# Optimization experiments

Measured on AMD Instinct MI355X. Metric: run time of the kernel, lower is better.

The kernel has to match this reference:

```python
import jax, jax.numpy as jnp
import numpy as np

BETA = 0.95
THR = 1.0
NUM_STEPS = 100
ALPHA = 2.0  # snntorch atan surrogate default

@jax.custom_vjp
def atan_spike(x):
    return (x > 0).astype(x.dtype)

def _as_fwd(x):
    return (x > 0).astype(x.dtype), x

def _as_bwd(x, g):
    return (g * (ALPHA / 2) / (1 + (jnp.pi / 2 * ALPHA * x) ** 2),)

atan_spike.defvjp(_as_fwd, _as_bwd)


def setup_inputs() -> dict:
    key = jax.random.key(0)
    ks = jax.random.split(key, 9)
    B = 16384
    SH, NH, CO, OUT = 1024, 1024, 256, 64
    s = 0.05
    return {
        "x": jax.random.normal(ks[0], (B, 105), jnp.float32),
        "snn_w1": jax.random.normal(ks[1], (SH, 5), jnp.float32) * s,
        "snn_b1": jnp.zeros((SH,), jnp.float32),
        "snn_w2": jax.random.normal(ks[2], (OUT, SH), jnp.float32) * s,
        "snn_b2": jnp.zeros((OUT,), jnp.float32),
        "nn_w1": jax.random.normal(ks[3], (NH, 5), jnp.float32) * s,
        "nn_b1": jnp.zeros((NH,), jnp.float32),
        "nn_w2": jax.random.normal(ks[4], (OUT, NH), jnp.float32) * s,
        "nn_b2": jnp.zeros((OUT,), jnp.float32),
        "conv_w": jax.random.normal(ks[5], (32, 1, 3), jnp.float32) * s,
        "conv_b": jnp.zeros((32,), jnp.float32),
        "cnn_fc_w": jax.random.normal(ks[6], (CO, 32 * 50), jnp.float32) * s,
        "cnn_fc_b": jnp.zeros((CO,), jnp.float32),
        "comb_w": jax.random.normal(ks[7], (OUT, 2 * OUT + CO), jnp.float32) * s,
        "comb_b": jnp.zeros((OUT,), jnp.float32),
    }


def _forward(x, snn_w1, snn_b1, snn_w2, snn_b2, nn_w1, nn_b1, nn_w2, nn_b2,
             conv_w, conv_b, cnn_fc_w, cnn_fc_b, comb_w, comb_b):
    feats = x[:, :5]                 # [B,5]
    wave = x[:, 5:][:, None, :]      # [B,1,100]
    B = x.shape[0]

    # ---- SNN branch (LIF, beta leak, subtract reset, threshold 1.0) ----
    cur1 = feats @ snn_w1.T + snn_b1  # input current is constant across steps

    def step(carry, _):
        mem1, spk1, mem2, spk2 = carry
        # reset term uses detached spike (snntorch mem_reset detaches)
        mem1 = BETA * mem1 + cur1 - jax.lax.stop_gradient(spk1) * THR
        spk1 = atan_spike(mem1 - THR)
        cur2 = spk1 @ snn_w2.T + snn_b2
        mem2 = BETA * mem2 + cur2 - jax.lax.stop_gradient(spk2) * THR
        spk2 = atan_spike(mem2 - THR)
        return (mem1, spk1, mem2, spk2), spk2

    z1 = jnp.zeros_like(cur1)
    z2 = jnp.zeros((B, snn_w2.shape[0]), cur1.dtype)
    _, spk_rec = jax.lax.scan(step, (z1, z1, z2, z2), None, length=NUM_STEPS)
    snn_out = spk_rec.mean(axis=0)   # [B,OUT]

    # ---- MLP branch ----
    nn_out = jax.nn.relu(feats @ nn_w1.T + nn_b1) @ nn_w2.T + nn_b2

    # ---- CNN branch ----
    c = jax.lax.conv_general_dilated(wave, conv_w, (1,), [(1, 1)],
                                     dimension_numbers=("NCW", "OIW", "NCW"))
    c = jax.nn.relu(c + conv_b[None, :, None])   # [B,32,100]
    c = c.reshape(B, 32, 50, 2).max(axis=-1)      # MaxPool1d(k=2,s=2)
    cnn_out = c.reshape(B, -1) @ cnn_fc_w.T + cnn_fc_b

    combined = jnp.concatenate([snn_out, nn_out, cnn_out], axis=1)
    return combined @ comb_w.T + comb_b


def reference(x, snn_w1, snn_b1, snn_w2, snn_b2, nn_w1, nn_b1, nn_w2, nn_b2,
              conv_w, conv_b, cnn_fc_w, cnn_fc_b, comb_w, comb_b):
    return _forward(x, snn_w1, snn_b1, snn_w2, snn_b2, nn_w1, nn_b1, nn_w2,
                    nn_b2, conv_w, conv_b, cnn_fc_w, cnn_fc_b, comb_w, comb_b)
```

## Files before the change

kernel.cpp:

```cpp
#include <hip/hip_runtime.h>

typedef __bf16 bf16x8_t __attribute__((ext_vector_type(8)));
typedef float f32x4_t __attribute__((ext_vector_type(4)));
typedef float f32x2_t __attribute__((ext_vector_type(2)));

#define NSTEPS 100
#define COMBF 51200u

static __device__ __forceinline__ unsigned short f2bfu(float v) {
  union { __bf16 h; unsigned short u; } c; c.h = (__bf16)v; return c.u;
}
static __device__ __forceinline__ unsigned int pack2bf(float a, float b) {
  return (unsigned)f2bfu(a) | ((unsigned)f2bfu(b) << 16);
}
union BF8U { unsigned int u[4]; bf16x8_t v; };

static __device__ __forceinline__ void pk_mul_ip(f32x2_t &a, f32x2_t b) {
  asm("v_pk_mul_f32 %0, %0, %1" : "+v"(a) : "v"(b));
}
static __device__ __forceinline__ void pk_add_ip(f32x2_t &a, f32x2_t b) {
  asm("v_pk_add_f32 %0, %0, %1" : "+v"(a) : "v"(b));
}

static __device__ __forceinline__ bf16x8_t bfrag_f32(const float* __restrict__ p, float s) {
  BF8U r;
#pragma unroll
  for (int i = 0; i < 4; ++i) r.u[i] = pack2bf(p[2*i]*s, p[2*i+1]*s);
  return r.v;
}

static __device__ __forceinline__ void comb_store(unsigned char* ldsp, int k, int row, float v) {
  *(unsigned short*)(ldsp + COMBF +
      (unsigned)((k >> 5)*1024 + (((k >> 3) & 3)*16 + row)*16 + (k & 7)*2)) = f2bfu(v);
}

__global__ __launch_bounds__(512, 2)
void hybrid_v6(const float* __restrict__ x,
               const float* __restrict__ snn_w1, const float* __restrict__ snn_b1,
               const float* __restrict__ snn_w2, const float* __restrict__ snn_b2,
               const float* __restrict__ nn_w1,  const float* __restrict__ nn_b1,
               const float* __restrict__ nn_w2,  const float* __restrict__ nn_b2,
               const float* __restrict__ conv_w, const float* __restrict__ conv_b,
               const float* __restrict__ fc_w,   const float* __restrict__ fc_b,
               const float* __restrict__ comb_w, const float* __restrict__ comb_b,
               const unsigned short* __restrict__ fcwb, int use_bf,
               float* __restrict__ out)
{
  __shared__ __align__(16) unsigned char lds[131072];
  const int tid  = threadIdx.x;
  const int w    = tid >> 6;
  const int l    = tid & 63;
  const int q    = l >> 4;
  const int m    = l & 15;
  const int row0 = blockIdx.x * 16;

  const int hi  = w >> 2;
  const int ntr = w & 3;
  const int rn  = ntr*16 + m;
  const int rA  = hi*4 + q;

  const float* xr = x + (row0 + m)*105;
  const float f0 = xr[0], f1 = xr[1], f2 = xr[2], f3 = xr[3], f4 = xr[4];
  const float b2l = snn_b2[rn];

  bf16x8_t bfr[4][4];
#pragma unroll
  for (int ci = 0; ci < 4; ++ci)
#pragma unroll
    for (int nt = 0; nt < 4; ++nt)
      bfr[ci][nt] = bfrag_f32(snn_w2 + (nt*16 + m)*1024 + (w*4 + ci)*32 + q*8, 1.f);

  f32x2_t c2[16], mem2[16];
  f32x2_t beta2; beta2.x = 0.95f; beta2.y = 0.95f;
  {
    const int kb = w*128 + q*8;
#pragma unroll
    for (int ci = 0; ci < 4; ++ci) {
      const float* wp = snn_w1 + (kb + ci*32)*5;
      float wa[40];
#pragma unroll
      for (int u2 = 0; u2 < 10; ++u2) {
        const float4 t4 = *(const float4*)(wp + u2*4);
        wa[u2*4+0] = t4.x; wa[u2*4+1] = t4.y; wa[u2*4+2] = t4.z; wa[u2*4+3] = t4.w;
      }
      float cc[8];
#pragma unroll
      for (int j = 0; j < 8; ++j)
        cc[j] = f0*wa[j*5] + f1*wa[j*5+1] + f2*wa[j*5+2] + f3*wa[j*5+3] + f4*wa[j*5+4]
              + snn_b1[kb + ci*32 + j];
#pragma unroll
      for (int jj = 0; jj < 4; ++jj) {
        f32x2_t t; t.x = cc[2*jj]; t.y = cc[2*jj+1];
        c2[ci*4+jj] = t;
        f32x2_t z; z.x = 0.f; z.y = 0.f;
        mem2[ci*4+jj] = z;
      }
    }
  }

  BF8U afr[4][4];
#pragma unroll
  for (int ci = 0; ci < 4; ++ci)
#pragma unroll
    for (int j = 0; j < 4; ++j) afr[3][ci].u[j] = 0u;

  auto lif_step = [&](int pi, int po) {
#pragma unroll
    for (int i = 0; i < 16; ++i) {
      const unsigned pw = afr[pi][i>>2].u[i&3];
      f32x2_t sn;
      sn.x = __uint_as_float((pw << 16) | 0x80000000u);
      sn.y = __uint_as_float((pw & 0x3F800000u) | 0x80000000u);
      pk_mul_ip(mem2[i], beta2);
      pk_add_ip(mem2[i], c2[i]);
      pk_add_ip(mem2[i], sn);
      const unsigned lo  = mem2[i].x > 1.f ? 0x3F80u     : 0u;
      const unsigned hi2 = mem2[i].y > 1.f ? 0x3F800000u : 0u;
      afr[po][i>>2].u[i&3] = lo | hi2;
    }
  };
  lif_step(3,0); lif_step(0,1); lif_step(1,2); lif_step(2,3);

  f32x2_t m2;     m2.x = 0.f;      m2.y = 0.f;
  f32x2_t s2neg;  s2neg.x = -0.0f; s2neg.y = -0.0f;
  f32x2_t cntneg; cntneg.x = 0.f;  cntneg.y = 0.f;
  f32x2_t sbias2; sbias2.x = b2l;  sbias2.y = b2l;

  const unsigned wbase = (unsigned)(w*4096 + (q&1)*2048 + (q>>1)*4 + m*8);
  const unsigned rbase = (unsigned)(rA*512 + rn*8);
  const f32x4_t z4 = {0.f, 0.f, 0.f, 0.f};

  auto reduce_lif2 = [&](f32x2_t v[8]) {
    pk_add_ip(v[0], v[1]); pk_add_ip(v[2], v[3]);
    pk_add_ip(v[4], v[5]); pk_add_ip(v[6], v[7]);
    pk_add_ip(v[0], v[2]); pk_add_ip(v[4], v[6]);
    pk_add_ip(v[0], v[4]);
    pk_add_ip(v[0], sbias2);
    pk_mul_ip(m2, beta2);
    pk_add_ip(m2, v[0]);
    pk_add_ip(m2, s2neg);
    s2neg.x = m2.x > 1.f ? -1.0f : -0.0f;
    s2neg.y = m2.y > 1.f ? -1.0f : -0.0f;
    pk_add_ip(cntneg, s2neg);
  };

#pragma unroll 1
  for (int ss = 0; ss < 25; ++ss) {
#pragma unroll
    for (int k = 0; k < 4; ++k) {
      f32x4_t acc[4] = {z4, z4, z4, z4};
#pragma unroll
      for (int ci = 0; ci < 4; ++ci)
#pragma unroll
        for (int nt = 0; nt < 4; ++nt)
          acc[nt] = __builtin_amdgcn_mfma_f32_16x16x32_bf16(afr[k][ci].v, bfr[ci][nt], acc[nt], 0,0,0);
      unsigned char* wp = lds + (unsigned)(k*32768) + wbase;
#pragma unroll
      for (int nt = 0; nt < 4; ++nt)
#pragma unroll
        for (int r = 0; r < 4; ++r)
          *(float*)(wp + (unsigned)(r*512 + nt*128)) = acc[nt][r];
    }
    __syncthreads();

    {
      const unsigned char* rp = lds + rbase;
      f32x2_t va[8], vb[8];
#pragma unroll
      for (int s = 0; s < 8; ++s) va[s] = *(const f32x2_t*)(rp + (unsigned)(s*4096));
#pragma unroll
      for (int s = 0; s < 8; ++s) vb[s] = *(const f32x2_t*)(rp + 32768u + (unsigned)(s*4096));
      if (ss < 24) { lif_step(3,0); lif_step(0,1); lif_step(1,2); lif_step(2,3); }
      reduce_lif2(va);
      reduce_lif2(vb);
#pragma unroll
      for (int s = 0; s < 8; ++s) va[s] = *(const f32x2_t*)(rp + 65536u + (unsigned)(s*4096));
#pragma unroll
      for (int s = 0; s < 8; ++s) vb[s] = *(const f32x2_t*)(rp + 98304u + (unsigned)(s*4096));
      reduce_lif2(va);
      reduce_lif2(vb);
    }
    __syncthreads();
  }

#pragma unroll
  for (int ci = 0; ci < 4; ++ci)
#pragma unroll
    for (int nt = 0; nt < 4; ++nt)
      bfr[ci][nt] = bfrag_f32(nn_w2 + (nt*16 + m)*1024 + (w*4 + ci)*32 + q*8, 1.f);
  {
    BF8U hfr[4];
    const int kb = w*128 + q*8;
#pragma unroll
    for (int ci = 0; ci < 4; ++ci) {
      const float* wp = nn_w1 + (kb + ci*32)*5;
      float wa[40];
#pragma unroll
      for (int u2 = 0; u2 < 10; ++u2) {
        const float4 t4 = *(const float4*)(wp + u2*4);
        wa[u2*4+0] = t4.x; wa[u2*4+1] = t4.y; wa[u2*4+2] = t4.z; wa[u2*4+3] = t4.w;
      }
      float hv[8];
#pragma unroll
      for (int j = 0; j < 8; ++j) {
        const float h = f0*wa[j*5] + f1*wa[j*5+1] + f2*wa[j*5+2] + f3*wa[j*5+3] + f4*wa[j*5+4]
                      + nn_b1[kb + ci*32 + j];
        hv[j] = fmaxf(h, 0.f);
      }
#pragma unroll
      for (int jj = 0; jj < 4; ++jj) hfr[ci].u[jj] = pack2bf(hv[2*jj], hv[2*jj+1]);
    }
    f32x4_t acc[4] = {z4, z4, z4, z4};
#pragma unroll
    for (int ci = 0; ci < 4; ++ci)
#pragma unroll
      for (int nt = 0; nt < 4; ++nt)
        acc[nt] = __builtin_amdgcn_mfma_f32_16x16x32_bf16(hfr[ci].v, bfr[ci][nt], acc[nt], 0,0,0);
#pragma unroll
    for (int nt = 0; nt < 4; ++nt)
#pragma unroll
      for (int r = 0; r < 4; ++r)
        *(float*)(lds + wbase + (unsigned)(r*512 + nt*128)) = acc[nt][r];
  }
  __syncthreads();
  {
    f32x2_t va[8];
    const unsigned char* rp = lds + rbase;
#pragma unroll
    for (int s = 0; s < 8; ++s) va[s] = *(const f32x2_t*)(rp + (unsigned)(s*4096));
    pk_add_ip(va[0], va[1]); pk_add_ip(va[2], va[3]);
    pk_add_ip(va[4], va[5]); pk_add_ip(va[6], va[7]);
    pk_add_ip(va[0], va[2]); pk_add_ip(va[4], va[6]);
    pk_add_ip(va[0], va[4]);
    const float nb = nn_b2[rn];
    f32x2_t nb2; nb2.x = nb; nb2.y = nb;
    pk_add_ip(va[0], nb2);
    comb_store(lds, rn,      rA,     cntneg.x * -0.0078125f);
    comb_store(lds, rn,      rA + 8, cntneg.y * -0.0078125f);
    comb_store(lds, 64 + rn, rA,     va[0].x);
    comb_store(lds, 64 + rn, rA + 8, va[0].y);
  }
  __syncthreads();

  {
    const int ch = tid >> 4;
    const float cw0 = conv_w[ch*3+0], cw1 = conv_w[ch*3+1], cw2 = conv_w[ch*3+2];
    const float cbb = conv_b[ch];
    const float* xw = xr + 5;
    float xm1 = 0.f, x0v = xw[0];
#pragma unroll 1
    for (int p = 0; p < 50; ++p) {
      const float xp1 = xw[2*p + 1];
      const float xp2 = (p < 49) ? xw[2*p + 2] : 0.f;
      const float av = cw0*xm1 + cw1*x0v + cw2*xp1 + cbb;
      const float bv = cw0*x0v + cw1*xp1 + cw2*xp2 + cbb;
      const float pv = fmaxf(fmaxf(av, 0.f), fmaxf(bv, 0.f));
      const int k = ch*50 + p;
      *(unsigned short*)(lds + (unsigned)((k>>5)*1024 + (((k>>3)&3)*16 + m)*16 + (k&7)*2)) = f2bfu(pv);
      xm1 = xp1; x0v = xp2;
    }
  }
  __syncthreads();

  {
    const int c0 = (w*2 + 0)*16 + m;
    const int c1 = (w*2 + 1)*16 + m;
    f32x4_t e0 = z4, o0 = z4, e1 = z4, o1 = z4;
    if (use_bf) {
#pragma unroll 2
      for (int kc = 0; kc < 50; kc += 2) {
        const bf16x8_t a0 = *(const bf16x8_t*)(lds + (unsigned)((kc*64 + l)*16));
        const bf16x8_t a1 = *(const bf16x8_t*)(lds + (unsigned)(((kc+1)*64 + l)*16));
        e0 = __builtin_amdgcn_mfma_f32_16x16x32_bf16(a0, *(const bf16x8_t*)(fcwb + c0*1600 + kc*32 + q*8), e0, 0,0,0);
        o0 = __builtin_amdgcn_mfma_f32_16x16x32_bf16(a1, *(const bf16x8_t*)(fcwb + c0*1600 + (kc+1)*32 + q*8), o0, 0,0,0);
        e1 = __builtin_amdgcn_mfma_f32_16x16x32_bf16(a0, *(const bf16x8_t*)(fcwb + c1*1600 + kc*32 + q*8), e1, 0,0,0);
        o1 = __builtin_amdgcn_mfma_f32_16x16x32_bf16(a1, *(const bf16x8_t*)(fcwb + c1*1600 + (kc+1)*32 + q*8), o1, 0,0,0);
      }
    } else {
#pragma unroll 2
      for (int kc = 0; kc < 50; kc += 2) {
        const bf16x8_t a0 = *(const bf16x8_t*)(lds + (unsigned)((kc*64 + l)*16));
        const bf16x8_t a1 = *(const bf16x8_t*)(lds + (unsigned)(((kc+1)*64 + l)*16));
        e0 = __builtin_amdgcn_mfma_f32_16x16x32_bf16(a0, bfrag_f32(fc_w + c0*1600 + kc*32 + q*8, 1.f), e0, 0,0,0);
        o0 = __builtin_amdgcn_mfma_f32_16x16x32_bf16(a1, bfrag_f32(fc_w + c0*1600 + (kc+1)*32 + q*8, 1.f), o0, 0,0,0);
        e1 = __builtin_amdgcn_mfma_f32_16x16x32_bf16(a0, bfrag_f32(fc_w + c1*1600 + kc*32 + q*8, 1.f), e1, 0,0,0);
        o1 = __builtin_amdgcn_mfma_f32_16x16x32_bf16(a1, bfrag_f32(fc_w + c1*1600 + (kc+1)*32 + q*8, 1.f), o1, 0,0,0);
      }
    }
    const float fb0 = fc_b[c0], fb1 = fc_b[c1];
#pragma unroll
    for (int r = 0; r < 4; ++r) {
      comb_store(lds, 128 + c0, q*4 + r, (e0[r] + o0[r]) + fb0);
      comb_store(lds, 128 + c1, q*4 + r, (e1[r] + o1[r]) + fb1);
    }
  }
  __syncthreads();

  if (w < 4) {
    const int cn = w*16 + m;
    f32x4_t oe = z4, oo = z4;
#pragma unroll
    for (int kc = 0; kc < 12; kc += 2) {
      const bf16x8_t a0 = *(const bf16x8_t*)(lds + COMBF + (unsigned)((kc*64 + l)*16));
      const bf16x8_t a1 = *(const bf16x8_t*)(lds + COMBF + (unsigned)(((kc+1)*64 + l)*16));
      const float s0 = (kc    < 2) ? 1.28f : 1.f;
      const float s1 = (kc+1 < 2) ? 1.28f : 1.f;
      oe = __builtin_amdgcn_mfma_f32_16x16x32_bf16(a0, bfrag_f32(comb_w + cn*384 + kc*32 + q*8, s0), oe, 0,0,0);
      oo = __builtin_amdgcn_mfma_f32_16x16x32_bf16(a1, bfrag_f32(comb_w + cn*384 + (kc+1)*32 + q*8, s1), oo, 0,0,0);
    }
    const float cb2 = comb_b[cn];
#pragma unroll
    for (int r = 0; r < 4; ++r)
      out[(row0 + q*4 + r)*64 + cn] = (oe[r] + oo[r]) + cb2;
  }
}

__global__ __launch_bounds__(256)
void fcw_to_bf16(const float* __restrict__ src, unsigned short* __restrict__ dst) {
  const int i = (blockIdx.x * 256 + threadIdx.x) * 4;
  const float4 v = *(const float4*)(src + i);
  ushort4 o;
  o.x = f2bfu(v.x); o.y = f2bfu(v.y); o.z = f2bfu(v.z); o.w = f2bfu(v.w);
  *(ushort4*)(dst + i) = o;
}

extern "C" void kernel_launch(void* const* d_in, const int* in_sizes, int n_in,
                              void* d_out, int out_size, void* d_ws, size_t ws_size,
                              hipStream_t stream) {
  const float* x       = (const float*)d_in[0];
  const float* snn_w1  = (const float*)d_in[1];
  const float* snn_b1  = (const float*)d_in[2];
  const float* snn_w2  = (const float*)d_in[3];
  const float* snn_b2  = (const float*)d_in[4];
  const float* nn_w1   = (const float*)d_in[5];
  const float* nn_b1   = (const float*)d_in[6];
  const float* nn_w2   = (const float*)d_in[7];
  const float* nn_b2   = (const float*)d_in[8];
  const float* conv_w  = (const float*)d_in[9];
  const float* conv_b  = (const float*)d_in[10];
  const float* fc_w    = (const float*)d_in[11];
  const float* fc_b    = (const float*)d_in[12];
  const float* comb_w  = (const float*)d_in[13];
  const float* comb_b  = (const float*)d_in[14];
  float* outp = (float*)d_out;

  const int rows = in_sizes[0] / 105;
  const int grid = rows / 16;

  const size_t fcw_elems = (size_t)in_sizes[11];
  const int use_bf = (ws_size >= fcw_elems * 2) ? 1 : 0;
  unsigned short* fcwb = (unsigned short*)d_ws;
  if (use_bf) {
    fcw_to_bf16<<<dim3((unsigned)(fcw_elems / 1024)), dim3(256), 0, stream>>>(fc_w, fcwb);
  }

  hybrid_v6<<<dim3(grid), dim3(512), 0, stream>>>(
      x, snn_w1, snn_b1, snn_w2, snn_b2,
      nn_w1, nn_b1, nn_w2, nn_b2,
      conv_w, conv_b, fc_w, fc_b, comb_w, comb_b,
      fcwb, use_bf, outp);
}
```

Baseline: 762.9 us.

## Interleave layer-1 LIF step with each MFMA step to cut register footprint

Replaces the four-deep buffer of precomputed layer-1 spike fragments with a single fragment set. The next LIF step now runs right after each step's MFMAs instead of four steps being batched in the reduction phase. Spike state is kept as negative float reset values and packed to bf16 with a perm instruction. This frees VGPRs and lets the VALU LIF work overlap the MFMA latency, but the inner k loop is no longer unrolled, which adds loop overhead and restricts scheduling.

```diff
diff --git a/kernel.cpp b/kernel.cpp
--- a/kernel.cpp
+++ b/kernel.cpp
@@ -35,7 +35,7 @@
 }
 
 __global__ __launch_bounds__(512, 2)
-void hybrid_v6(const float* __restrict__ x,
+void hybrid_v7(const float* __restrict__ x,
                const float* __restrict__ snn_w1, const float* __restrict__ snn_b1,
                const float* __restrict__ snn_w2, const float* __restrict__ snn_b2,
                const float* __restrict__ nn_w1,  const float* __restrict__ nn_b1,
@@ -70,7 +70,7 @@
     for (int nt = 0; nt < 4; ++nt)
       bfr[ci][nt] = bfrag_f32(snn_w2 + (nt*16 + m)*1024 + (w*4 + ci)*32 + q*8, 1.f);
 
-  f32x2_t c2[16], mem2[16];
+  f32x2_t c2[16], mem2[16], spneg2[16];
   f32x2_t beta2; beta2.x = 0.95f; beta2.y = 0.95f;
   {
     const int kb = w*128 + q*8;
@@ -94,32 +94,29 @@
         c2[ci*4+jj] = t;
         f32x2_t z; z.x = 0.f; z.y = 0.f;
         mem2[ci*4+jj] = z;
-      }
-    }
-  }
-
-  BF8U afr[4][4];
-#pragma unroll
-  for (int ci = 0; ci < 4; ++ci)
-#pragma unroll
-    for (int j = 0; j < 4; ++j) afr[3][ci].u[j] = 0u;
-
-  auto lif_step = [&](int pi, int po) {
+        f32x2_t nz; nz.x = -0.0f; nz.y = -0.0f;
+        spneg2[ci*4+jj] = nz;
+      }
+    }
+  }
+
+  BF8U afr[4];
+  auto lif_step = [&]() {
 #pragma unroll
     for (int i = 0; i < 16; ++i) {
-      const unsigned pw = afr[pi][i>>2].u[i&3];
-      f32x2_t sn;
-      sn.x = __uint_as_float((pw << 16) | 0x80000000u);
-      sn.y = __uint_as_float((pw & 0x3F800000u) | 0x80000000u);
       pk_mul_ip(mem2[i], beta2);
       pk_add_ip(mem2[i], c2[i]);
-      pk_add_ip(mem2[i], sn);
-      const unsigned lo  = mem2[i].x > 1.f ? 0x3F80u     : 0u;
-      const unsigned hi2 = mem2[i].y > 1.f ? 0x3F800000u : 0u;
-      afr[po][i>>2].u[i&3] = lo | hi2;
+      pk_add_ip(mem2[i], spneg2[i]);
+      f32x2_t sn;
+      sn.x = mem2[i].x > 1.f ? -1.0f : -0.0f;
+      sn.y = mem2[i].y > 1.f ? -1.0f : -0.0f;
+      spneg2[i] = sn;
+      afr[i>>2].u[i&3] =
+          __builtin_amdgcn_perm(__float_as_uint(sn.y), __float_as_uint(sn.x), 0x07060302u)
+          & 0x3F803F80u;
     }
   };
-  lif_step(3,0); lif_step(0,1); lif_step(1,2); lif_step(2,3);
+  lif_step();
 
   f32x2_t m2;     m2.x = 0.f;      m2.y = 0.f;
   f32x2_t s2neg;  s2neg.x = -0.0f; s2neg.y = -0.0f;
@@ -146,14 +143,15 @@
 
 #pragma unroll 1
   for (int ss = 0; ss < 25; ++ss) {
-#pragma unroll
+#pragma unroll 1
     for (int k = 0; k < 4; ++k) {
       f32x4_t acc[4] = {z4, z4, z4, z4};
 #pragma unroll
       for (int ci = 0; ci < 4; ++ci)
 #pragma unroll
         for (int nt = 0; nt < 4; ++nt)
-          acc[nt] = __builtin_amdgcn_mfma_f32_16x16x32_bf16(afr[k][ci].v, bfr[ci][nt], acc[nt], 0,0,0);
+          acc[nt] = __builtin_amdgcn_mfma_f32_16x16x32_bf16(afr[ci].v, bfr[ci][nt], acc[nt], 0,0,0);
+      if (ss*4 + k < NSTEPS - 1) lif_step();
       unsigned char* wp = lds + (unsigned)(k*32768) + wbase;
 #pragma unroll
       for (int nt = 0; nt < 4; ++nt)
@@ -170,7 +168,6 @@
       for (int s = 0; s < 8; ++s) va[s] = *(const f32x2_t*)(rp + (unsigned)(s*4096));
 #pragma unroll
       for (int s = 0; s < 8; ++s) vb[s] = *(const f32x2_t*)(rp + 32768u + (unsigned)(s*4096));
-      if (ss < 24) { lif_step(3,0); lif_step(0,1); lif_step(1,2); lif_step(2,3); }
       reduce_lif2(va);
       reduce_lif2(vb);
 #pragma unroll
@@ -354,7 +351,7 @@
     fcw_to_bf16<<<dim3((unsigned)(fcw_elems / 1024)), dim3(256), 0, stream>>>(fc_w, fcwb);
   }
 
-  hybrid_v6<<<dim3(grid), dim3(512), 0, stream>>>(
+  hybrid_v7<<<dim3(grid), dim3(512), 0, stream>>>(
       x, snn_w1, snn_b1, snn_w2, snn_b2,
       nn_w1, nn_b1, nn_w2, nn_b2,
       conv_w, conv_b, fc_w, fc_b, comb_w, comb_b,
```

After: 700.8 us. -8.1%, faster.

## Process two 16-row tiles per block and software-pipeline the SNN timestep loop

Applied to the files above, without the earlier changes.

Each block now handles 32 batch rows as two independent 16-row tiles (A and B), halving the grid. The SNN loop is restructured so each phase issues one timestep's MFMAs for both tiles, interleaves the next layer-1 LIF update and the reduction of the previous step's partials from a double-buffered LDS region, and uses one barrier per step instead of batching four steps with two barriers. This interleaving is meant to hide MFMA and LDS latency behind independent work and to reuse the weight fragments in registers across twice as many rows. In exchange it roughly doubles per-thread state (membrane and current registers), which raises register pressure and risks spills at the 512x2 launch bound. It also halves the number of blocks, which lowers parallelism across CUs.

```diff
diff --git a/kernel.cpp b/kernel.cpp
--- a/kernel.cpp
+++ b/kernel.cpp
@@ -5,7 +5,13 @@
 typedef float f32x2_t __attribute__((ext_vector_type(2)));
 
 #define NSTEPS 100
-#define COMBF 51200u
+#define APB0 0u
+#define APB1 32768u
+#define TB   65536u
+#define POOLA 0u
+#define POOLB 51200u
+#define COMBA 102400u
+#define COMBB 114688u
 
 static __device__ __forceinline__ unsigned short f2bfu(float v) {
   union { __bf16 h; unsigned short u; } c; c.h = (__bf16)v; return c.u;
@@ -29,22 +35,23 @@
   return r.v;
 }
 
-static __device__ __forceinline__ void comb_store(unsigned char* ldsp, int k, int row, float v) {
-  *(unsigned short*)(ldsp + COMBF +
+static __device__ __forceinline__ void comb_store(unsigned char* ldsp, unsigned base,
+                                                  int k, int row, float v) {
+  *(unsigned short*)(ldsp + base +
       (unsigned)((k >> 5)*1024 + (((k >> 3) & 3)*16 + row)*16 + (k & 7)*2)) = f2bfu(v);
 }
 
 __global__ __launch_bounds__(512, 2)
-void hybrid_v6(const float* __restrict__ x,
-               const float* __restrict__ snn_w1, const float* __restrict__ snn_b1,
-               const float* __restrict__ snn_w2, const float* __restrict__ snn_b2,
-               const float* __restrict__ nn_w1,  const float* __restrict__ nn_b1,
-               const float* __restrict__ nn_w2,  const float* __restrict__ nn_b2,
-               const float* __restrict__ conv_w, const float* __restrict__ conv_b,
-               const float* __restrict__ fc_w,   const float* __restrict__ fc_b,
-               const float* __restrict__ comb_w, const float* __restrict__ comb_b,
-               const unsigned short* __restrict__ fcwb, int use_bf,
-               float* __restrict__ out)
+void hybrid_v11(const float* __restrict__ x,
+                const float* __restrict__ snn_w1, const float* __restrict__ snn_b1,
+                const float* __restrict__ snn_w2, const float* __restrict__ snn_b2,
+                const float* __restrict__ nn_w1,  const float* __restrict__ nn_b1,
+                const float* __restrict__ nn_w2,  const float* __restrict__ nn_b2,
+                const float* __restrict__ conv_w, const float* __restrict__ conv_b,
+                const float* __restrict__ fc_w,   const float* __restrict__ fc_b,
+                const float* __restrict__ comb_w, const float* __restrict__ comb_b,
+                const unsigned short* __restrict__ fcwb, int use_bf,
+                float* __restrict__ out)
 {
   __shared__ __align__(16) unsigned char lds[131072];
   const int tid  = threadIdx.x;
@@ -52,15 +59,13 @@
   const int l    = tid & 63;
   const int q    = l >> 4;
   const int m    = l & 15;
-  const int row0 = blockIdx.x * 16;
+  const int row0 = blockIdx.x * 32;
 
   const int hi  = w >> 2;
   const int ntr = w & 3;
   const int rn  = ntr*16 + m;
   const int rA  = hi*4 + q;
 
-  const float* xr = x + (row0 + m)*105;
-  const float f0 = xr[0], f1 = xr[1], f2 = xr[2], f3 = xr[3], f4 = xr[4];
   const float b2l = snn_b2[rn];
 
   bf16x8_t bfr[4][4];
@@ -70,118 +75,177 @@
     for (int nt = 0; nt < 4; ++nt)
       bfr[ci][nt] = bfrag_f32(snn_w2 + (nt*16 + m)*1024 + (w*4 + ci)*32 + q*8, 1.f);
 
-  f32x2_t c2[16], mem2[16];
+  f32x2_t c2A[16], mem2A[16], c2B[16], mem2B[16];
   f32x2_t beta2; beta2.x = 0.95f; beta2.y = 0.95f;
   {
     const int kb = w*128 + q*8;
-#pragma unroll
-    for (int ci = 0; ci < 4; ++ci) {
-      const float* wp = snn_w1 + (kb + ci*32)*5;
-      float wa[40];
-#pragma unroll
-      for (int u2 = 0; u2 < 10; ++u2) {
-        const float4 t4 = *(const float4*)(wp + u2*4);
-        wa[u2*4+0] = t4.x; wa[u2*4+1] = t4.y; wa[u2*4+2] = t4.z; wa[u2*4+3] = t4.w;
-      }
-      float cc[8];
-#pragma unroll
-      for (int j = 0; j < 8; ++j)
-        cc[j] = f0*wa[j*5] + f1*wa[j*5+1] + f2*wa[j*5+2] + f3*wa[j*5+3] + f4*wa[j*5+4]
-              + snn_b1[kb + ci*32 + j];
-#pragma unroll
-      for (int jj = 0; jj < 4; ++jj) {
-        f32x2_t t; t.x = cc[2*jj]; t.y = cc[2*jj+1];
-        c2[ci*4+jj] = t;
-        f32x2_t z; z.x = 0.f; z.y = 0.f;
-        mem2[ci*4+jj] = z;
-      }
-    }
-  }
-
-  BF8U afr[4][4];
+    {
+      const float* xr = x + (row0 + m)*105;
+      const float f0 = xr[0], f1 = xr[1], f2 = xr[2], f3 = xr[3], f4 = xr[4];
+#pragma unroll
+      for (int ci = 0; ci < 4; ++ci) {
+        const float* wp = snn_w1 + (kb + ci*32)*5;
+        float wa[40];
+#pragma unroll
+        for (int u2 = 0; u2 < 10; ++u2) {
+          const float4 t4 = *(const float4*)(wp + u2*4);
+          wa[u2*4+0] = t4.x; wa[u2*4+1] = t4.y; wa[u2*4+2] = t4.z; wa[u2*4+3] = t4.w;
+        }
+        float cc[8];
+#pragma unroll
+        for (int j = 0; j < 8; ++j)
+          cc[j] = f0*wa[j*5] + f1*wa[j*5+1] + f2*wa[j*5+2] + f3*wa[j*5+3] + f4*wa[j*5+4]
+                + snn_b1[kb + ci*32 + j];
+#pragma unroll
+        for (int jj = 0; jj < 4; ++jj) {
+          f32x2_t t; t.x = cc[2*jj]; t.y = cc[2*jj+1];
+          c2A[ci*4+jj] = t;
+          f32x2_t z; z.x = 0.f; z.y = 0.f;
+          mem2A[ci*4+jj] = z;
+        }
+      }
+    }
+    {
+      const float* xr = x + (row0 + 16 + m)*105;
+      const float f0 = xr[0], f1 = xr[1], f2 = xr[2], f3 = xr[3], f4 = xr[4];
+#pragma unroll
+      for (int ci = 0; ci < 4; ++ci) {
+        const float* wp = snn_w1 + (kb + ci*32)*5;
+        float wa[40];
+#pragma unroll
+        for (int u2 = 0; u2 < 10; ++u2) {
+          const float4 t4 = *(const float4*)(wp + u2*4);
+          wa[u2*4+0] = t4.x; wa[u2*4+1] = t4.y; wa[u2*4+2] = t4.z; wa[u2*4+3] = t4.w;
+        }
+        float cc[8];
+#pragma unroll
+        for (int j = 0; j < 8; ++j)
+          cc[j] = f0*wa[j*5] + f1*wa[j*5+1] + f2*wa[j*5+2] + f3*wa[j*5+3] + f4*wa[j*5+4]
+                + snn_b1[kb + ci*32 + j];
+#pragma unroll
+        for (int jj = 0; jj < 4; ++jj) {
+          f32x2_t t; t.x = cc[2*jj]; t.y = cc[2*jj+1];
+          c2B[ci*4+jj] = t;
+          f32x2_t z; z.x = 0.f; z.y = 0.f;
+          mem2B[ci*4+jj] = z;
+        }
+      }
+    }
+  }
+
+  BF8U afrA[4], afrB[4];
 #pragma unroll
   for (int ci = 0; ci < 4; ++ci)
 #pragma unroll
-    for (int j = 0; j < 4; ++j) afr[3][ci].u[j] = 0u;
-
-  auto lif_step = [&](int pi, int po) {
+    for (int j = 0; j < 4; ++j) { afrA[ci].u[j] = 0u; afrB[ci].u[j] = 0u; }
+
+  auto lif_stepA = [&]() {
 #pragma unroll
     for (int i = 0; i < 16; ++i) {
-      const unsigned pw = afr[pi][i>>2].u[i&3];
+      const unsigned pw = afrA[i>>2].u[i&3];
       f32x2_t sn;
       sn.x = __uint_as_float((pw << 16) | 0x80000000u);
       sn.y = __uint_as_float((pw & 0x3F800000u) | 0x80000000u);
-      pk_mul_ip(mem2[i], beta2);
-      pk_add_ip(mem2[i], c2[i]);
-      pk_add_ip(mem2[i], sn);
-      const unsigned lo  = mem2[i].x > 1.f ? 0x3F80u     : 0u;
-      const unsigned hi2 = mem2[i].y > 1.f ? 0x3F800000u : 0u;
-      afr[po][i>>2].u[i&3] = lo | hi2;
+      pk_mul_ip(mem2A[i], beta2);
+      pk_add_ip(mem2A[i], c2A[i]);
+      pk_add_ip(mem2A[i], sn);
+      const unsigned lo  = mem2A[i].x > 1.f ? 0x3F80u     : 0u;
+      const unsigned hi2 = mem2A[i].y > 1.f ? 0x3F800000u : 0u;
+      afrA[i>>2].u[i&3] = lo | hi2;
     }
   };
-  lif_step(3,0); lif_step(0,1); lif_step(1,2); lif_step(2,3);
-
-  f32x2_t m2;     m2.x = 0.f;      m2.y = 0.f;
-  f32x2_t s2neg;  s2neg.x = -0.0f; s2neg.y = -0.0f;
-  f32x2_t cntneg; cntneg.x = 0.f;  cntneg.y = 0.f;
-  f32x2_t sbias2; sbias2.x = b2l;  sbias2.y = b2l;
+  auto lif_stepB = [&]() {
+#pragma unroll
+    for (int i = 0; i < 16; ++i) {
+      const unsigned pw = afrB[i>>2].u[i&3];
+      f32x2_t sn;
+      sn.x = __uint_as_float((pw << 16) | 0x80000000u);
+      sn.y = __uint_as_float((pw & 0x3F800000u) | 0x80000000u);
+      pk_mul_ip(mem2B[i], beta2);
+      pk_add_ip(mem2B[i], c2B[i]);
+      pk_add_ip(mem2B[i], sn);
+      const unsigned lo  = mem2B[i].x > 1.f ? 0x3F80u     : 0u;
+      const unsigned hi2 = mem2B[i].y > 1.f ? 0x3F800000u : 0u;
+      afrB[i>>2].u[i&3] = lo | hi2;
+    }
+  };
+  lif_stepA(); lif_stepB();
+
+  f32x2_t m2A, s2nA, cntA, m2B, s2nB, cntB, sbias2;
+  m2A.x = 0.f; m2A.y = 0.f;  s2nA.x = -0.0f; s2nA.y = -0.0f;  cntA.x = 0.f; cntA.y = 0.f;
+  m2B.x = 0.f; m2B.y = 0.f;  s2nB.x = -0.0f; s2nB.y = -0.0f;  cntB.x = 0.f; cntB.y = 0.f;
+  sbias2.x = b2l; sbias2.y = b2l;
 
   const unsigned wbase = (unsigned)(w*4096 + (q&1)*2048 + (q>>1)*4 + m*8);
   const unsigned rbase = (unsigned)(rA*512 + rn*8);
   const f32x4_t z4 = {0.f, 0.f, 0.f, 0.f};
 
-  auto reduce_lif2 = [&](f32x2_t v[8]) {
+  auto tree8 = [&](unsigned off) -> f32x2_t {
+    const unsigned char* rp = lds + off + rbase;
+    f32x2_t v[8];
+#pragma unroll
+    for (int s = 0; s < 8; ++s) v[s] = *(const f32x2_t*)(rp + (unsigned)(s*4096));
     pk_add_ip(v[0], v[1]); pk_add_ip(v[2], v[3]);
     pk_add_ip(v[4], v[5]); pk_add_ip(v[6], v[7]);
     pk_add_ip(v[0], v[2]); pk_add_ip(v[4], v[6]);
     pk_add_ip(v[0], v[4]);
-    pk_add_ip(v[0], sbias2);
+    return v[0];
+  };
+  auto l2up = [&](f32x2_t t, f32x2_t &m2, f32x2_t &s2n, f32x2_t &cnt) {
+    pk_add_ip(t, sbias2);
     pk_mul_ip(m2, beta2);
-    pk_add_ip(m2, v[0]);
-    pk_add_ip(m2, s2neg);
-    s2neg.x = m2.x > 1.f ? -1.0f : -0.0f;
-    s2neg.y = m2.y > 1.f ? -1.0f : -0.0f;
-    pk_add_ip(cntneg, s2neg);
+    pk_add_ip(m2, t);
+    pk_add_ip(m2, s2n);
+    s2n.x = m2.x > 1.f ? -1.0f : -0.0f;
+    s2n.y = m2.y > 1.f ? -1.0f : -0.0f;
+    pk_add_ip(cnt, s2n);
   };
 
-#pragma unroll 1
-  for (int ss = 0; ss < 25; ++ss) {
-#pragma unroll
-    for (int k = 0; k < 4; ++k) {
+  auto phase = [&](unsigned cur, unsigned prv, bool doRead, bool doLif) {
+    {
       f32x4_t acc[4] = {z4, z4, z4, z4};
 #pragma unroll
       for (int ci = 0; ci < 4; ++ci)
 #pragma unroll
         for (int nt = 0; nt < 4; ++nt)
-          acc[nt] = __builtin_amdgcn_mfma_f32_16x16x32_bf16(afr[k][ci].v, bfr[ci][nt], acc[nt], 0,0,0);
-      unsigned char* wp = lds + (unsigned)(k*32768) + wbase;
+          acc[nt] = __builtin_amdgcn_mfma_f32_16x16x32_bf16(afrA[ci].v, bfr[ci][nt], acc[nt], 0,0,0);
+      if (doLif) lif_stepA();
+      unsigned char* wp = lds + cur + wbase;
 #pragma unroll
       for (int nt = 0; nt < 4; ++nt)
 #pragma unroll
         for (int r = 0; r < 4; ++r)
           *(float*)(wp + (unsigned)(r*512 + nt*128)) = acc[nt][r];
+      if (doRead) l2up(tree8(prv), m2A, s2nA, cntA);
+    }
+    {
+      f32x4_t acc[4] = {z4, z4, z4, z4};
+#pragma unroll
+      for (int ci = 0; ci < 4; ++ci)
+#pragma unroll
+        for (int nt = 0; nt < 4; ++nt)
+          acc[nt] = __builtin_amdgcn_mfma_f32_16x16x32_bf16(afrB[ci].v, bfr[ci][nt], acc[nt], 0,0,0);
+      if (doLif) lif_stepB();
+      unsigned char* wp = lds + cur + TB + wbase;
+#pragma unroll
+      for (int nt = 0; nt < 4; ++nt)
+#pragma unroll
+        for (int r = 0; r < 4; ++r)
+          *(float*)(wp + (unsigned)(r*512 + nt*128)) = acc[nt][r];
+      if (doRead) l2up(tree8(prv + TB), m2B, s2nB, cntB);
     }
     __syncthreads();
-
-    {
-      const unsigned char* rp = lds + rbase;
-      f32x2_t va[8], vb[8];
-#pragma unroll
-      for (int s = 0; s < 8; ++s) va[s] = *(const f32x2_t*)(rp + (unsigned)(s*4096));
-#pragma unroll
-      for (int s = 0; s < 8; ++s) vb[s] = *(const f32x2_t*)(rp + 32768u + (unsigned)(s*4096));
-      if (ss < 24) { lif_step(3,0); lif_step(0,1); lif_step(1,2); lif_step(2,3); }
-      reduce_lif2(va);
-      reduce_lif2(vb);
-#pragma unroll
-      for (int s = 0; s < 8; ++s) va[s] = *(const f32x2_t*)(rp + 65536u + (unsigned)(s*4096));
-#pragma unroll
-      for (int s = 0; s < 8; ++s) vb[s] = *(const f32x2_t*)(rp + 98304u + (unsigned)(s*4096));
-      reduce_lif2(va);
-      reduce_lif2(vb);
-    }
-    __syncthreads();
-  }
+  };
+
+#pragma unroll 1
+  for (int tt = 0; tt < NSTEPS; tt += 2) {
+    phase(APB0, APB1, tt > 0, true);
+    phase(APB1, APB0, true,  tt + 1 < NSTEPS - 1);
+  }
+
+  int zz = 0; asm volatile("" : "+v"(zz));
+  const float* xrA = x + ((row0 + m)*105 + zz);
+  const float* xrB = xrA + 16*105;
 
 #pragma unroll
   for (int ci = 0; ci < 4; ++ci)
@@ -189,56 +253,97 @@
     for (int nt = 0; nt < 4; ++nt)
       bfr[ci][nt] = bfrag_f32(nn_w2 + (nt*16 + m)*1024 + (w*4 + ci)*32 + q*8, 1.f);
   {
-    BF8U hfr[4];
+    l2up(tree8(APB1),      m2A, s2nA, cntA);
+    l2up(tree8(APB1 + TB), m2B, s2nB, cntB);
+
     const int kb = w*128 + q*8;
-#pragma unroll
-    for (int ci = 0; ci < 4; ++ci) {
-      const float* wp = nn_w1 + (kb + ci*32)*5;
-      float wa[40];
-#pragma unroll
-      for (int u2 = 0; u2 < 10; ++u2) {
-        const float4 t4 = *(const float4*)(wp + u2*4);
-        wa[u2*4+0] = t4.x; wa[u2*4+1] = t4.y; wa[u2*4+2] = t4.z; wa[u2*4+3] = t4.w;
-      }
-      float hv[8];
-#pragma unroll
-      for (int j = 0; j < 8; ++j) {
-        const float h = f0*wa[j*5] + f1*wa[j*5+1] + f2*wa[j*5+2] + f3*wa[j*5+3] + f4*wa[j*5+4]
-                      + nn_b1[kb + ci*32 + j];
-        hv[j] = fmaxf(h, 0.f);
-      }
-#pragma unroll
-      for (int jj = 0; jj < 4; ++jj) hfr[ci].u[jj] = pack2bf(hv[2*jj], hv[2*jj+1]);
-    }
-    f32x4_t acc[4] = {z4, z4, z4, z4};
-#pragma unroll
-    for (int ci = 0; ci < 4; ++ci)
+    {
+      const float f0 = xrA[0], f1 = xrA[1], f2 = xrA[2], f3 = xrA[3], f4 = xrA[4];
+      BF8U hfr[4];
+#pragma unroll
+      for (int ci = 0; ci < 4; ++ci) {
+        const float* wp = nn_w1 + (kb + ci*32)*5;
+        float wa[40];
+#pragma unroll
+        for (int u2 = 0; u2 < 10; ++u2) {
+          const float4 t4 = *(const float4*)(wp + u2*4);
+          wa[u2*4+0] = t4.x; wa[u2*4+1] = t4.y; wa[u2*4+2] = t4.z; wa[u2*4+3] = t4.w;
+        }
+        float hv[8];
+#pragma unroll
+        for (int j = 0; j < 8; ++j) {
+          const float h = f0*wa[j*5] + f1*wa[j*5+1] + f2*wa[j*5+2] + f3*wa[j*5+3] + f4*wa[j*5+4]
+                        + nn_b1[kb + ci*32 + j];
+          hv[j] = fmaxf(h, 0.f);
+        }
+#pragma unroll
+        for (int jj = 0; jj < 4; ++jj) hfr[ci].u[jj] = pack2bf(hv[2*jj], hv[2*jj+1]);
+      }
+      f32x4_t acc[4] = {z4, z4, z4, z4};
+#pragma unroll
+      for (int ci = 0; ci < 4; ++ci)
+#pragma unroll
+        for (int nt = 0; nt < 4; ++nt)
+          acc[nt] = __builtin_amdgcn_mfma_f32_16x16x32_bf16(hfr[ci].v, bfr[ci][nt], acc[nt], 0,0,0);
+      unsigned char* wp2 = lds + APB0 + wbase;
 #pragma unroll
       for (int nt = 0; nt < 4; ++nt)
-        acc[nt] = __builtin_amdgcn_mfma_f32_16x16x32_bf16(hfr[ci].v, bfr[ci][nt], acc[nt], 0,0,0);
-#pragma unroll
-    for (int nt = 0; nt < 4; ++nt)
-#pragma unroll
-      for (int r = 0; r < 4; ++r)
-        *(float*)(lds + wbase + (unsigned)(r*512 + nt*128)) = acc[nt][r];
+#pragma unroll
+        for (int r = 0; r < 4; ++r)
+          *(float*)(wp2 + (unsigned)(r*512 + nt*128)) = acc[nt][r];
+    }
+    {
+      const float f0 = xrB[0], f1 = xrB[1], f2 = xrB[2], f3 = xrB[3], f4 = xrB[4];
+      BF8U hfr[4];
+#pragma unroll
+      for (int ci = 0; ci < 4; ++ci) {
+        const float* wp = nn_w1 + (kb + ci*32)*5;
+        float wa[40];
+#pragma unroll
+        for (int u2 = 0; u2 < 10; ++u2) {
+          const float4 t4 = *(const float4*)(wp + u2*4);
+          wa[u2*4+0] = t4.x; wa[u2*4+1] = t4.y; wa[u2*4+2] = t4.z; wa[u2*4+3] = t4.w;
+        }
+        float hv[8];
+#pragma unroll
+        for (int j = 0; j < 8; ++j) {
+          const float h = f0*wa[j*5] + f1*wa[j*5+1] + f2*wa[j*5+2] + f3*wa[j*5+3] + f4*wa[j*5+4]
+                        + nn_b1[kb + ci*32 + j];
+          hv[j] = fmaxf(h, 0.f);
+        }
+#pragma unroll
+        for (int jj = 0; jj < 4; ++jj) hfr[ci].u[jj] = pack2bf(hv[2*jj], hv[2*jj+1]);
+      }
+      f32x4_t acc[4] = {z4, z4, z4, z4};
+#pragma unroll
+      for (int ci = 0; ci < 4; ++ci)
+#pragma unroll
+        for (int nt = 0; nt < 4; ++nt)
+          acc[nt] = __builtin_amdgcn_mfma_f32_16x16x32_bf16(hfr[ci].v, bfr[ci][nt], acc[nt], 0,0,0);
+      unsigned char* wp2 = lds + APB0 + TB + wbase;
+#pragma unroll
+      for (int nt = 0; nt < 4; ++nt)
+#pragma unroll
+        for (int r = 0; r < 4; ++r)
+          *(float*)(wp2 + (unsigned)(r*512 + nt*128)) = acc[nt][r];
+    }
   }
   __syncthreads();
   {
-    f32x2_t va[8];
-    const unsigned char* rp = lds + rbase;
-#pragma unroll
-    for (int s = 0; s < 8; ++s) va[s] = *(const f32x2_t*)(rp + (unsigned)(s*4096));
-    pk_add_ip(va[0], va[1]); pk_add_ip(va[2], va[3]);
-    pk_add_ip(va[4], va[5]); pk_add_ip(va[6], va[7]);
-    pk_add_ip(va[0], va[2]); pk_add_ip(va[4], va[6]);
-    pk_add_ip(va[0], va[4]);
+    f32x2_t nA = tree8(APB0);
+    f32x2_t nB = tree8(APB0 + TB);
     const float nb = nn_b2[rn];
     f32x2_t nb2; nb2.x = nb; nb2.y = nb;
-    pk_add_ip(va[0], nb2);
-    comb_store(lds, rn,      rA,     cntneg.x * -0.0078125f);
-    comb_store(lds, rn,      rA + 8, cntneg.y * -0.0078125f);
-    comb_store(lds, 64 + rn, rA,     va[0].x);
-    comb_store(lds, 64 + rn, rA + 8, va[0].y);
+    pk_add_ip(nA, nb2);
+    pk_add_ip(nB, nb2);
+    comb_store(lds, COMBA, rn,      rA,     cntA.x * -0.0078125f);
+    comb_store(lds, COMBA, rn,      rA + 8, cntA.y * -0.0078125f);
+    comb_store(lds, COMBA, 64 + rn, rA,     nA.x);
+    comb_store(lds, COMBA, 64 + rn, rA + 8, nA.y);
+    comb_store(lds, COMBB, rn,      rA,     cntB.x * -0.0078125f);
+    comb_store(lds, COMBB, rn,      rA + 8, cntB.y * -0.0078125f);
+    comb_store(lds, COMBB, 64 + rn, rA,     nB.x);
+    comb_store(lds, COMBB, 64 + rn, rA + 8, nB.y);
   }
   __syncthreads();
 
@@ -246,18 +351,37 @@
     const int ch = tid >> 4;
     const float cw0 = conv_w[ch*3+0], cw1 = conv_w[ch*3+1], cw2 = conv_w[ch*3+2];
     const float cbb = conv_b[ch];
-    const float* xw = xr + 5;
-    float xm1 = 0.f, x0v = xw[0];
+    {
+      const float* xw = xrA + 5;
+      float xm1 = 0.f, x0v = xw[0];
 #pragma unroll 1
-    for (int p = 0; p < 50; ++p) {
-      const float xp1 = xw[2*p + 1];
-      const float xp2 = (p < 49) ? xw[2*p + 2] : 0.f;
-      const float av = cw0*xm1 + cw1*x0v + cw2*xp1 + cbb;
-      const float bv = cw0*x0v + cw1*xp1 + cw2*xp2 + cbb;
-      const float pv = fmaxf(fmaxf(av, 0.f), fmaxf(bv, 0.f));
-      const int k = ch*50 + p;
-      *(unsigned short*)(lds + (unsigned)((k>>5)*1024 + (((k>>3)&3)*16 + m)*16 + (k&7)*2)) = f2bfu(pv);
-      xm1 = xp1; x0v = xp2;
+      for (int p = 0; p < 50; ++p) {
+        const float xp1 = xw[2*p + 1];
+        const float xp2 = (p < 49) ? xw[2*p + 2] : 0.f;
+        const float av = cw0*xm1 + cw1*x0v + cw2*xp1 + cbb;
+        const float bv = cw0*x0v + cw1*xp1 + cw2*xp2 + cbb;
+        const float pv = fmaxf(fmaxf(av, 0.f), fmaxf(bv, 0.f));
+        const int k = ch*50 + p;
+        *(unsigned short*)(lds + POOLA +
+            (unsigned)((k>>5)*1024 + (((k>>3)&3)*16 + m)*16 + (k&7)*2)) = f2bfu(pv);
+        xm1 = xp1; x0v = xp2;
+      }
+    }
+    {
+      const float* xw = xrB + 5;
+      float xm1 = 0.f, x0v = xw[0];
+#pragma unroll 1
+      for (int p = 0; p < 50; ++p) {
+        const float xp1 = xw[2*p + 1];
+        const float xp2 = (p < 49) ? xw[2*p + 2] : 0.f;
+        const float av = cw0*xm1 + cw1*x0v + cw2*xp1 + cbb;
+        const float bv = cw0*x0v + cw1*xp1 + cw2*xp2 + cbb;
+        const float pv = fmaxf(fmaxf(av, 0.f), fmaxf(bv, 0.f));
+        const int k = ch*50 + p;
+        *(unsigned short*)(lds + POOLB +
+            (unsigned)((k>>5)*1024 + (((k>>3)&3)*16 + m)*16 + (k&7)*2)) = f2bfu(pv);
+        xm1 = xp1; x0v = xp2;
+      }
     }
   }
   __syncthreads();
@@ -265,44 +389,69 @@
   {
     const int c0 = (w*2 + 0)*16 + m;
     const int c1 = (w*2 + 1)*16 + m;
-    f32x4_t e0 = z4, o0 = z4, e1 = z4, o1 = z4;
+    f32x4_t e0A = z4, o0A = z4, e1A = z4, o1A = z4;
+    f32x4_t e0B = z4, o0B = z4, e1B = z4, o1B = z4;
     if (use_bf) {
-#pragma unroll 2
+#pragma unroll 1
       for (int kc = 0; kc < 50; kc += 2) {
-        const bf16x8_t a0 = *(const bf16x8_t*)(lds + (unsigned)((kc*64 + l)*16));
-        const bf16x8_t a1 = *(const bf16x8_t*)(lds + (unsigned)(((kc+1)*64 + l)*16));
-        e0 = __builtin_amdgcn_mfma_f32_16x16x32_bf16(a0, *(const bf16x8_t*)(fcwb + c0*1600 + kc*32 + q*8), e0, 0,0,0);
-        o0 = __builtin_amdgcn_mfma_f32_16x16x32_bf16(a1, *(const bf16x8_t*)(fcwb + c0*1600 + (kc+1)*32 + q*8), o0, 0,0,0);
-        e1 = __builtin_amdgcn_mfma_f32_16x16x32_bf16(a0, *(const bf16x8_t*)(fcwb + c1*1600 + kc*32 + q*8), e1, 0,0,0);
-        o1 = __builtin_amdgcn_mfma_f32_16x16x32_bf16(a1, *(const bf16x8_t*)(fcwb + c1*1600 + (kc+1)*32 + q*8), o1, 0,0,0);
+        const bf16x8_t a0A = *(const bf16x8_t*)(lds + POOLA + (unsigned)((kc*64 + l)*16));
+        const bf16x8_t a1A = *(const bf16x8_t*)(lds + POOLA + (unsigned)(((kc+1)*64 + l)*16));
+        const bf16x8_t a0B = *(const bf16x8_t*)(lds + POOLB + (unsigned)((kc*64 + l)*16));
+        const bf16x8_t a1B = *(const bf16x8_t*)(lds + POOLB + (unsigned)(((kc+1)*64 + l)*16));
+        const bf16x8_t w00 = *(const bf16x8_t*)(fcwb + c0*1600 + kc*32 + q*8);
+        const bf16x8_t w01 = *(const bf16x8_t*)(fcwb + c0*1600 + (kc+1)*32 + q*8);
+        const bf16x8_t w10 = *(const bf16x8_t*)(fcwb + c1*1600 + kc*32 + q*8);
+        const bf16x8_t w11 = *(const bf16x8_t*)(fcwb + c1*1600 + (kc+1)*32 + q*8);
+        e0A = __builtin_amdgcn_mfma_f32_16x16x32_bf16(a0A, w00, e0A, 0,0,0);
+        o0A = __builtin_amdgcn_mfma_f32_16x16x32_bf16(a1A, w01, o0A, 0,0,0);
+        e1A = __builtin_amdgcn_mfma_f32_16x16x32_bf16(a0A, w10, e1A, 0,0,0);
+        o1A = __builtin_amdgcn_mfma_f32_16x16x32_bf16(a1A, w11, o1A, 0,0,0);
+        e0B = __builtin_amdgcn_mfma_f32_16x16x32_bf16(a0B, w00, e0B, 0,0,0);
+        o0B = __builtin_amdgcn_mfma_f32_16x16x32_bf16(a1B, w01, o0B, 0,0,0);
+        e1B = __builtin_amdgcn_mfma_f32_16x16x32_bf16(a0B, w10, e1B, 0,0,0);
+        o1B = __builtin_amdgcn_mfma_f32_16x16x32_bf16(a1B, w11, o1B, 0,0,0);
       }
     } else {
-#pragma unroll 2
+#pragma unroll 1
       for (int kc = 0; kc < 50; kc += 2) {
-        const bf16x8_t a0 = *(const bf16x8_t*)(lds + (unsigned)((kc*64 + l)*16));
-        const bf16x8_t a1 = *(const bf16x8_t*)(lds + (unsigned)(((kc+1)*64 + l)*16));
-        e0 = __builtin_amdgcn_mfma_f32_16x16x32_bf16(a0, bfrag_f32(fc_w + c0*1600 + kc*32 + q*8, 1.f), e0, 0,0,0);
-        o0 = __builtin_amdgcn_mfma_f32_16x16x32_bf16(a1, bfrag_f32(fc_w + c0*1600 + (kc+1)*32 + q*8, 1.f), o0, 0,0,0);
-        e1 = __builtin_amdgcn_mfma_f32_16x16x32_bf16(a0, bfrag_f32(fc_w + c1*1600 + kc*32 + q*8, 1.f), e1, 0,0,0);
-        o1 = __builtin_amdgcn_mfma_f32_16x16x32_bf16(a1, bfrag_f32(fc_w + c1*1600 + (kc+1)*32 + q*8, 1.f), o1, 0,0,0);
+        const bf16x8_t a0A = *(const bf16x8_t*)(lds + POOLA + (unsigned)((kc*64 + l)*16));
+        const bf16x8_t a1A = *(const bf16x8_t*)(lds + POOLA + (unsigned)(((kc+1)*64 + l)*16));
+        const bf16x8_t a0B = *(const bf16x8_t*)(lds + POOLB + (unsigned)((kc*64 + l)*16));
+        const bf16x8_t a1B = *(const bf16x8_t*)(lds + POOLB + (unsigned)(((kc+1)*64 + l)*16));
+        const bf16x8_t w00 = bfrag_f32(fc_w + c0*1600 + kc*32 + q*8, 1.f);
+        const bf16x8_t w01 = bfrag_f32(fc_w + c0*1600 + (kc+1)*32 + q*8, 1.f);
+        const bf16x8_t w10 = bfrag_f32(fc_w + c1*1600 + kc*32 + q*8, 1.f);
+        const bf16x8_t w11 = bfrag_f32(fc_w + c1*1600 + (kc+1)*32 + q*8, 1.f);
+        e0A = __builtin_amdgcn_mfma_f32_16x16x32_bf16(a0A, w00, e0A, 0,0,0);
+        o0A = __builtin_amdgcn_mfma_f32_16x16x32_bf16(a1A, w01, o0A, 0,0,0);
+        e1A = __builtin_amdgcn_mfma_f32_16x16x32_bf16(a0A, w10, e1A, 0,0,0);
+        o1A = __builtin_amdgcn_mfma_f32_16x16x32_bf16(a1A, w11, o1A, 0,0,0);
+        e0B = __builtin_amdgcn_mfma_f32_16x16x32_bf16(a0B, w00, e0B, 0,0,0);
+        o0B = __builtin_amdgcn_mfma_f32_16x16x32_bf16(a1B, w01, o0B, 0,0,0);
+        e1B = __builtin_amdgcn_mfma_f32_16x16x32_bf16(a0B, w10, e1B, 0,0,0);
+        o1B = __builtin_amdgcn_mfma_f32_16x16x32_bf16(a1B, w11, o1B, 0,0,0);
       }
     }
     const float fb0 = fc_b[c0], fb1 = fc_b[c1];
 #pragma unroll
     for (int r = 0; r < 4; ++r) {
-      comb_store(lds, 128 + c0, q*4 + r, (e0[r] + o0[r]) + fb0);
-      comb_store(lds, 128 + c1, q*4 + r, (e1[r] + o1[r]) + fb1);
+      comb_store(lds, COMBA, 128 + c0, q*4 + r, (e0A[r] + o0A[r]) + fb0);
+      comb_store(lds, COMBA, 128 + c1, q*4 + r, (e1A[r] + o1A[r]) + fb1);
+      comb_store(lds, COMBB, 128 + c0, q*4 + r, (e0B[r] + o0B[r]) + fb0);
+      comb_store(lds, COMBB, 128 + c1, q*4 + r, (e1B[r] + o1B[r]) + fb1);
     }
   }
   __syncthreads();
 
-  if (w < 4) {
-    const int cn = w*16 + m;
+  {
+    const int tb = w >> 2;
+    const unsigned cb = tb ? COMBB : COMBA;
+    const int cn = (w & 3)*16 + m;
     f32x4_t oe = z4, oo = z4;
 #pragma unroll
     for (int kc = 0; kc < 12; kc += 2) {
-      const bf16x8_t a0 = *(const bf16x8_t*)(lds + COMBF + (unsigned)((kc*64 + l)*16));
-      const bf16x8_t a1 = *(const bf16x8_t*)(lds + COMBF + (unsigned)(((kc+1)*64 + l)*16));
+      const bf16x8_t a0 = *(const bf16x8_t*)(lds + cb + (unsigned)((kc*64 + l)*16));
+      const bf16x8_t a1 = *(const bf16x8_t*)(lds + cb + (unsigned)(((kc+1)*64 + l)*16));
       const float s0 = (kc    < 2) ? 1.28f : 1.f;
       const float s1 = (kc+1 < 2) ? 1.28f : 1.f;
       oe = __builtin_amdgcn_mfma_f32_16x16x32_bf16(a0, bfrag_f32(comb_w + cn*384 + kc*32 + q*8, s0), oe, 0,0,0);
@@ -311,7 +460,7 @@
     const float cb2 = comb_b[cn];
 #pragma unroll
     for (int r = 0; r < 4; ++r)
-      out[(row0 + q*4 + r)*64 + cn] = (oe[r] + oo[r]) + cb2;
+      out[(row0 + tb*16 + q*4 + r)*64 + cn] = (oe[r] + oo[r]) + cb2;
   }
 }
 
@@ -345,7 +494,7 @@
   float* outp = (float*)d_out;
 
   const int rows = in_sizes[0] / 105;
-  const int grid = rows / 16;
+  const int grid = rows / 32;
 
   const size_t fcw_elems = (size_t)in_sizes[11];
   const int use_bf = (ws_size >= fcw_elems * 2) ? 1 : 0;
@@ -354,7 +503,7 @@
     fcw_to_bf16<<<dim3((unsigned)(fcw_elems / 1024)), dim3(256), 0, stream>>>(fc_w, fcwb);
   }
 
-  hybrid_v6<<<dim3(grid), dim3(512), 0, stream>>>(
+  hybrid_v11<<<dim3(grid), dim3(512), 0, stream>>>(
       x, snn_w1, snn_b1, snn_w2, snn_b2,
       nn_w1, nn_b1, nn_w2, nn_b2,
       conv_w, conv_b, fc_w, fc_b, comb_w, comb_b,
```

Result: slower. 1.119 ms (+46.7%).
